# Performance work log

Hardware: AMD Instinct MI355X
Metric: run time of the kernel (lower is better)

Reference implementation:

```python
import math
import jax, jax.numpy as jnp
import numpy as np

D_MODEL, STATE_DIM, SEQ_L = 256, 64, 8192


def setup_inputs() -> dict:
    key = jax.random.key(0)
    ks = jax.random.split(key, 6)
    d, N = D_MODEL, STATE_DIM
    s = 1.0 / math.sqrt(N)
    return {
        "Lambda_re": jax.random.normal(ks[0], (d, N), jnp.float32),
        "Lambda_im": jax.random.normal(ks[1], (d, N), jnp.float32),
        "P_re": jax.random.normal(ks[2], (d, N), jnp.float32) * s,
        "P_im": jax.random.normal(ks[3], (d, N), jnp.float32) * s,
        "B_re": jax.random.normal(ks[4], (d, N), jnp.float32) * s,
        "B_im": jnp.zeros((d, N), jnp.float32),
        "log_dt": jax.random.uniform(ks[5], (d,), jnp.float32,
                                     math.log(1e-3), math.log(0.1)),
        "D": jnp.zeros((d,), jnpp := jnp.float32) if False else jnp.zeros((d,), jnp.float32),
        "L": SEQ_L,
    }


def reference(Lambda_re, Lambda_im, P_re, P_im, B_re, B_im, log_dt, D, L):
    # NPLR / Cauchy-Woodbury S4 kernel (learn_cd=False -> C = B, D is a zero buffer)
    Lam = (-jax.nn.softplus(Lambda_re) + 1j * Lambda_im).astype(jnp.complex64)  # [d, N]
    P = (P_re + 1j * P_im).astype(jnp.complex64)                                # [d, N]
    B = (B_re + 1j * B_im).astype(jnp.complex64)                                # [d, N]
    dt = jnp.exp(log_dt)                                                        # [d]

    k = jnp.arange(L)
    z = jnp.exp((-2j * jnp.pi / L) * k).astype(jnp.complex64)                   # [L] roots of unity
    eps = jnp.finfo(jnp.float32).eps
    denom_z = 1.0 + z
    denom_z = jnp.where(jnp.abs(denom_z) < eps, jnp.complex64(eps), denom_z)

    # Bilinear-transform frequencies g: [d, L] complex
    g = (2.0 / dt)[:, None] * ((1.0 - z) / denom_z)[None, :]

    # Cauchy resolvent R: [d, L, N] complex (the dominant intermediate)
    R = 1.0 / (g[:, :, None] - Lam[:, None, :])

    Pc, Bc = jnp.conj(P), jnp.conj(B)
    PRB = jnp.einsum('dn,dln,dn->dl', Pc, R, B)
    PRP = jnp.einsum('dn,dln,dn->dl', Pc, R, P)
    BRB = jnp.einsum('dn,dln,dn->dl', Bc, R, B)
    BRP = jnp.einsum('dn,dln,dn->dl', Bc, R, P)

    # Woodbury rank-1 correction, then undo the bilinear prefactor
    K_hat = (2.0 / denom_z)[None, :] * (BRB - BRP * PRB / (1.0 + PRP))          # [d, L]
    K = jnp.fft.ifft(K_hat, n=L, axis=-1).real.astype(jnp.float32)
    return (K, D)
```

## Files before the change

### kernel.cpp

```cpp
#include <hip/hip_runtime.h>
#include <math.h>

#ifndef M_PI
#define M_PI 3.14159265358979323846
#endif

#define DMODEL 256
#define NSTATE 64
#define LSEQ   8192
#define INVL   (1.0f/8192.0f)

#define OFF_TW  0
#define OFF_DN  (6144*8)
#define OFF_CDT (OFF_DN + DMODEL*NSTATE*48)
#define OFF_XY  (OFF_CDT + 1024)
#define WS_NEED ((size_t)OFF_XY + (size_t)DMODEL*LSEQ*8)

__device__ __forceinline__ float sin_rev(float r) {
#if __has_builtin(__builtin_amdgcn_sinf)
  return __builtin_amdgcn_sinf(r);
#else
  return __sinf(r * 6.283185307179586f);
#endif
}
__device__ __forceinline__ float cos_rev(float r) {
#if __has_builtin(__builtin_amdgcn_cosf)
  return __builtin_amdgcn_cosf(r);
#else
  return __cosf(r * 6.283185307179586f);
#endif
}

__device__ __forceinline__ float2 cmul(float2 a, float2 b) {
  return make_float2(a.x*b.x - a.y*b.y, a.x*b.y + a.y*b.x);
}

__device__ __forceinline__ float2 woodbury(float2 S1, float2 S2, float2 S3,
                                           float2 S4, float T) {
  float nr = (S1.x*S1.x - S1.y*S1.y) + (S2.x*S2.x - S2.y*S2.y);
  float ni = 2.0f*(S1.x*S1.y + S2.x*S2.y);
  float dr = 1.0f + S3.x, di = S3.y;
  float inv = __builtin_amdgcn_rcpf(fmaf(dr, dr, di*di));
  float qr = (nr*dr + ni*di) * inv;
  float qi = (ni*dr - nr*di) * inv;
  float vr = S4.x - qr, vi = S4.y - qi;
  return make_float2((vr - T*vi)*INVL, (vi + T*vr)*INVL);
}

__device__ __forceinline__ void radix4(float2& x0, float2& x1, float2& x2, float2& x3,
                                       float2 w1, float2 w2, float2 w3) {
  const float2 t1 = cmul(w1, x1);
  const float2 t2 = cmul(w2, x2);
  const float2 t3 = cmul(w3, x3);
  const float2 u0 = make_float2(x0.x + t2.x, x0.y + t2.y);
  const float2 u1 = make_float2(x0.x - t2.x, x0.y - t2.y);
  const float2 u2 = make_float2(t1.x + t3.x, t1.y + t3.y);
  const float2 vv = make_float2(t1.x - t3.x, t1.y - t3.y);
  x0 = make_float2(u0.x + u2.x, u0.y + u2.y);
  x1 = make_float2(u1.x - vv.y, u1.y + vv.x);
  x2 = make_float2(u0.x - u2.x, u0.y - u2.y);
  x3 = make_float2(u1.x + vv.y, u1.y - vv.x);
}

__device__ __forceinline__ float4 cauchy_pair(const float4* __restrict__ dnp,
                                              const float c, const int b) {
  const unsigned p = (unsigned)(2*b);
  const unsigned r = __brev(p) >> 19;
  const int kA = (int)((r & 0x1000u) | ((r & 0x0555u) << 1) | ((r & 0x0AAAu) >> 1));
  const float rev = (float)kA * (1.0f/16384.0f);
  const float sA = sin_rev(rev), cA = cos_rev(rev);
  float TA = sA * __builtin_amdgcn_rcpf(cA);
  float TB = -cA * __builtin_amdgcn_rcpf(sA);
  TA = fminf(fmaxf(TA, -1e7f), 1e7f);
  TB = fminf(fmaxf(TB, -1e7f), 1e7f);
  const float gA = c * TA, gB = c * TB;

  float2 s1a={0,0}, s2a={0,0}, s3a={0,0}, s4a={0,0};
  float2 s1b={0,0}, s2b={0,0}, s3b={0,0}, s4b={0,0};
#pragma unroll 2
  for (int n = 0; n < NSTATE; ++n) {
    const float4 q0 = dnp[3*n];
    const float4 q1 = dnp[3*n+1];
    const float4 q2 = dnp[3*n+2];
    {
      const float dim = q0.x - gA;
      const float inv = __builtin_amdgcn_rcpf(fmaf(dim, dim, q0.y));
      const float v = dim * inv;
      s1a.x = fmaf(q0.z, inv, s1a.x);  s1a.y = fmaf(q1.z, v, s1a.y);
      s2a.x = fmaf(q0.w, inv, s2a.x);  s2a.y = fmaf(q1.w, v, s2a.y);
      s3a.x = fmaf(q1.x, inv, s3a.x);  s3a.y = fmaf(q2.x, v, s3a.y);
      s4a.x = fmaf(q1.y, inv, s4a.x);  s4a.y = fmaf(q2.y, v, s4a.y);
    }
    {
      const float dim = q0.x - gB;
      const float inv = __builtin_amdgcn_rcpf(fmaf(dim, dim, q0.y));
      const float v = dim * inv;
      s1b.x = fmaf(q0.z, inv, s1b.x);  s1b.y = fmaf(q1.z, v, s1b.y);
      s2b.x = fmaf(q0.w, inv, s2b.x);  s2b.y = fmaf(q1.w, v, s2b.y);
      s3b.x = fmaf(q1.x, inv, s3b.x);  s3b.y = fmaf(q2.x, v, s3b.y);
      s4b.x = fmaf(q1.y, inv, s4b.x);  s4b.y = fmaf(q2.y, v, s4b.y);
    }
  }
  const float2 KA = woodbury(s1a, s2a, s3a, s4a, TA);
  const float2 KB = woodbury(s1b, s2b, s3b, s4b, TB);
  return make_float4(KA.x + KB.x, KA.y + KB.y, KA.x - KB.x, KA.y - KB.y);
}

__global__ __launch_bounds__(256) void precompute_kernel(
    const float* __restrict__ Lre, const float* __restrict__ Lim,
    const float* __restrict__ Pre, const float* __restrict__ Pim,
    const float* __restrict__ Bre, const float* __restrict__ Bim,
    const float* __restrict__ log_dt, char* __restrict__ ws)
{
  const int t = blockIdx.x * blockDim.x + threadIdx.x;
  float2* tw  = (float2*)(ws + OFF_TW);
  float4* dn  = (float4*)(ws + OFF_DN);
  float*  cdt = (float*)(ws + OFF_CDT);

  if (t < 6144) {
    double th = (2.0 * M_PI / (double)LSEQ) * (double)t;
    double s, c; sincos(th, &s, &c);
    tw[t] = make_float2((float)c, (float)s);
  }
  {
    float lre = Lre[t], lim = Lim[t];
    float pre = Pre[t], pim = Pim[t];
    float bre = Bre[t], bim = Bim[t];
    float sp = fmaxf(lre, 0.0f) + log1pf(expf(-fabsf(lre)));
    float w1r = pre*bre + pim*bim;
    float w1i = pre*bim - pim*bre;
    float w2  = pre*pre + pim*pim;
    float w3  = bre*bre + bim*bim;
    dn[3*t]   = make_float4(lim, sp*sp, w1r*sp, w1i*sp);
    dn[3*t+1] = make_float4(w2*sp, w3*sp, w1r, w1i);
    dn[3*t+2] = make_float4(w2, w3, 0.0f, 0.0f);
  }
  if (t < DMODEL) cdt[t] = 2.0f * expf(-log_dt[t]);
}

__global__ __launch_bounds__(512, 8) void cauchyfft_kernel(
    const float4* __restrict__ dn_all, const float* __restrict__ cdt,
    const float2* __restrict__ tw, float2* __restrict__ xy_ws)
{
  __shared__ __align__(16) float2 xy[2048];
  const int d   = blockIdx.x >> 2;
  const int seg = blockIdx.x & 3;
  const int t   = threadIdx.x;
  const float c = cdt[d];
  const float4* dnp = dn_all + (size_t)d * (3*NSTATE);

#pragma unroll
  for (int pass = 0; pass < 2; ++pass) {
    const int bl = t + (pass << 9);
    ((float4*)xy)[bl] = cauchy_pair(dnp, c, (seg << 10) + bl);
  }
  __syncthreads();

#pragma unroll
  for (int s = 0; s < 4; ++s) {
    const int h = 2 << (2*s);
    const int twsh = 10 - 2*s;
    const int pos = t & (h - 1);
    const int i0 = ((t >> (1 + 2*s)) << (3 + 2*s)) + pos;
    const int ti = pos << twsh;
    float2 x0 = xy[i0], x1 = xy[i0 + h], x2 = xy[i0 + 2*h], x3 = xy[i0 + 3*h];
    radix4(x0, x1, x2, x3, tw[ti], tw[2*ti], tw[3*ti]);
    xy[i0] = x0; xy[i0 + h] = x1; xy[i0 + 2*h] = x2; xy[i0 + 3*h] = x3;
    __syncthreads();
  }

  {
    const int ti = t << 2;
    float2 x0 = xy[t], x1 = xy[t + 512], x2 = xy[t + 1024], x3 = xy[t + 1536];
    radix4(x0, x1, x2, x3, tw[ti], tw[2*ti], tw[3*ti]);
    float2* xg = xy_ws + (size_t)d * LSEQ + (seg << 11);
    xg[t] = x0; xg[t + 512] = x1; xg[t + 1024] = x2; xg[t + 1536] = x3;
  }
}

__global__ __launch_bounds__(256) void finish_kernel(
    const float2* __restrict__ xy_ws, const float2* __restrict__ tw,
    const float* __restrict__ Din, float* __restrict__ out)
{
  const int d   = blockIdx.x >> 3;
  const int pos = ((blockIdx.x & 7) << 8) + threadIdx.x;
  const float2* xr = xy_ws + (size_t)d * LSEQ;
  const float2 x0 = xr[pos];
  const float2 x1 = xr[pos + 2048];
  const float2 x2 = xr[pos + 4096];
  const float2 x3 = xr[pos + 6144];
  const float2 w1 = tw[pos], w2 = tw[2*pos], w3 = tw[3*pos];
  const float t1x = w1.x*x1.x - w1.y*x1.y, t1y = w1.x*x1.y + w1.y*x1.x;
  const float t2x = w2.x*x2.x - w2.y*x2.y;
  const float t3x = w3.x*x3.x - w3.y*x3.y, t3y = w3.x*x3.y + w3.y*x3.x;
  const float u0 = x0.x + t2x, u1 = x0.x - t2x;
  const float u2 = t1x + t3x, vy = t1y - t3y;
  float* orow = out + (size_t)d * LSEQ;
  orow[pos]        = u0 + u2;
  orow[pos + 2048] = u1 - vy;
  orow[pos + 4096] = u0 - u2;
  orow[pos + 6144] = u1 + vy;

  if (blockIdx.x == 0) out[(size_t)DMODEL * LSEQ + threadIdx.x] =
      (threadIdx.x < DMODEL) ? Din[threadIdx.x] : 0.0f;
}

__global__ __launch_bounds__(1024) void fused_kernel(
    const float4* __restrict__ dn_all, const float* __restrict__ cdt,
    const float2* __restrict__ tw, const float* __restrict__ Din,
    float* __restrict__ out)
{
  __shared__ __align__(16) float2 xy[LSEQ];
  const int d = blockIdx.x;
  const int t = threadIdx.x;
  const float c = cdt[d];
  const float4* dnp = dn_all + (size_t)d * (3*NSTATE);

  for (int j = 0; j < 4; ++j) {
    const int b = t + (j << 10);
    ((float4*)xy)[b] = cauchy_pair(dnp, c, b);
  }
  __syncthreads();

#pragma unroll
  for (int s = 0; s < 6; ++s) {
    const int h = 2 << (2*s);
    const int twsh = 10 - 2*s;
#pragma unroll
    for (int j = 0; j < 2; ++j) {
      const int bb = t + (j << 10);
      const int pos = bb & (h - 1);
      const int i0 = ((bb >> (1 + 2*s)) << (3 + 2*s)) + pos;
      const int ti = pos << twsh;
      float2 x0 = xy[i0], x1 = xy[i0 + h], x2 = xy[i0 + 2*h], x3 = xy[i0 + 3*h];
      radix4(x0, x1, x2, x3, tw[ti], tw[2*ti], tw[3*ti]);
      xy[i0] = x0; xy[i0 + h] = x1; xy[i0 + 2*h] = x2; xy[i0 + 3*h] = x3;
    }
    __syncthreads();
  }

  float* orow = out + (size_t)d * LSEQ;
  for (int i = t; i < LSEQ; i += 1024) orow[i] = xy[i].x;
  if (d == 0 && t < DMODEL) out[(size_t)DMODEL * LSEQ + t] = Din[t];
}

extern "C" void kernel_launch(void* const* d_in, const int* in_sizes, int n_in,
                              void* d_out, int out_size, void* d_ws, size_t ws_size,
                              hipStream_t stream)
{
  const float* Lre    = (const float*)d_in[0];
  const float* Lim    = (const float*)d_in[1];
  const float* Pre    = (const float*)d_in[2];
  const float* Pim    = (const float*)d_in[3];
  const float* Bre    = (const float*)d_in[4];
  const float* Bim    = (const float*)d_in[5];
  const float* log_dt = (const float*)d_in[6];
  const float* Din    = (const float*)d_in[7];
  float* out = (float*)d_out;
  char* ws = (char*)d_ws;

  hipLaunchKernelGGL(precompute_kernel, dim3(64), dim3(256), 0, stream,
                     Lre, Lim, Pre, Pim, Bre, Bim, log_dt, ws);

  if (ws_size >= WS_NEED) {
    hipLaunchKernelGGL(cauchyfft_kernel, dim3(DMODEL * 4), dim3(512), 0, stream,
                       (const float4*)(ws + OFF_DN), (const float*)(ws + OFF_CDT),
                       (const float2*)(ws + OFF_TW), (float2*)(ws + OFF_XY));
    hipLaunchKernelGGL(finish_kernel, dim3(DMODEL * 8), dim3(256), 0, stream,
                       (const float2*)(ws + OFF_XY), (const float2*)(ws + OFF_TW),
                       Din, out);
  } else {
    hipLaunchKernelGGL(fused_kernel, dim3(DMODEL), dim3(1024), 0, stream,
                       (const float4*)(ws + OFF_DN), (const float*)(ws + OFF_CDT),
                       (const float2*)(ws + OFF_TW), Din, out);
  }
}
```

Measured before the change: 128.0 us.

## Fuse both Cauchy passes into one n-loop and swizzle LDS FFT indices

The two per-thread Cauchy evaluations are merged into a single loop over the state dimension, so each dn float4 load is reused for four frequency points instead of two. This halves the global/L1 loads of the dn table and exposes more independent rcp/FMA chains. An XOR swizzle is also applied to the shared-memory FFT buffer indices to cut LDS bank conflicts in the strided radix-4 stages. The cost is higher register pressure from sixteen accumulators, which may lower occupancy under the 512x8 launch bound.

After: 131.3 us. 1.03x slower.

```diff
diff --git a/kernel.cpp b/kernel.cpp
--- a/kernel.cpp
+++ b/kernel.cpp
@@ -15,6 +15,8 @@
 #define OFF_CDT (OFF_DN + DMODEL*NSTATE*48)
 #define OFF_XY  (OFF_CDT + 1024)
 #define WS_NEED ((size_t)OFF_XY + (size_t)DMODEL*LSEQ*8)
+
+#define SWZ(i) ((i) ^ (((i) >> 4) & 14))
 
 __device__ __forceinline__ float sin_rev(float r) {
 #if __has_builtin(__builtin_amdgcn_sinf)
@@ -62,19 +64,25 @@
   x3 = make_float2(u1.x + vv.y, u1.y - vv.x);
 }
 
-__device__ __forceinline__ float4 cauchy_pair(const float4* __restrict__ dnp,
-                                              const float c, const int b) {
+__device__ __forceinline__ void pair_setup(const float c, const int b,
+                                           float& TA, float& TB,
+                                           float& gA, float& gB) {
   const unsigned p = (unsigned)(2*b);
   const unsigned r = __brev(p) >> 19;
   const int kA = (int)((r & 0x1000u) | ((r & 0x0555u) << 1) | ((r & 0x0AAAu) >> 1));
   const float rev = (float)kA * (1.0f/16384.0f);
   const float sA = sin_rev(rev), cA = cos_rev(rev);
-  float TA = sA * __builtin_amdgcn_rcpf(cA);
-  float TB = -cA * __builtin_amdgcn_rcpf(sA);
+  TA = sA * __builtin_amdgcn_rcpf(cA);
+  TB = -cA * __builtin_amdgcn_rcpf(sA);
   TA = fminf(fmaxf(TA, -1e7f), 1e7f);
   TB = fminf(fmaxf(TB, -1e7f), 1e7f);
-  const float gA = c * TA, gB = c * TB;
-
+  gA = c * TA; gB = c * TB;
+}
+
+__device__ __forceinline__ float4 cauchy_pair(const float4* __restrict__ dnp,
+                                              const float c, const int b) {
+  float TA, TB, gA, gB;
+  pair_setup(c, b, TA, TB, gA, gB);
   float2 s1a={0,0}, s2a={0,0}, s3a={0,0}, s4a={0,0};
   float2 s1b={0,0}, s2b={0,0}, s3b={0,0}, s4b={0,0};
 #pragma unroll 2
@@ -149,10 +157,52 @@
   const float c = cdt[d];
   const float4* dnp = dn_all + (size_t)d * (3*NSTATE);
 
-#pragma unroll
-  for (int pass = 0; pass < 2; ++pass) {
-    const int bl = t + (pass << 9);
-    ((float4*)xy)[bl] = cauchy_pair(dnp, c, (seg << 10) + bl);
+  float TA[2], TB[2], gA[2], gB[2];
+  float2 s1[2][2], s2[2][2], s3[2][2], s4[2][2];
+#pragma unroll
+  for (int j = 0; j < 2; ++j) {
+    pair_setup(c, (seg << 10) + t + (j << 9), TA[j], TB[j], gA[j], gB[j]);
+    s1[j][0]=make_float2(0,0); s2[j][0]=make_float2(0,0);
+    s3[j][0]=make_float2(0,0); s4[j][0]=make_float2(0,0);
+    s1[j][1]=make_float2(0,0); s2[j][1]=make_float2(0,0);
+    s3[j][1]=make_float2(0,0); s4[j][1]=make_float2(0,0);
+  }
+
+#pragma unroll 2
+  for (int n = 0; n < NSTATE; ++n) {
+    const float4 q0 = dnp[3*n];
+    const float4 q1 = dnp[3*n+1];
+    const float4 q2 = dnp[3*n+2];
+#pragma unroll
+    for (int j = 0; j < 2; ++j) {
+      {
+        const float dim = q0.x - gA[j];
+        const float inv = __builtin_amdgcn_rcpf(fmaf(dim, dim, q0.y));
+        const float v = dim * inv;
+        s1[j][0].x = fmaf(q0.z, inv, s1[j][0].x);  s1[j][0].y = fmaf(q1.z, v, s1[j][0].y);
+        s2[j][0].x = fmaf(q0.w, inv, s2[j][0].x);  s2[j][0].y = fmaf(q1.w, v, s2[j][0].y);
+        s3[j][0].x = fmaf(q1.x, inv, s3[j][0].x);  s3[j][0].y = fmaf(q2.x, v, s3[j][0].y);
+        s4[j][0].x = fmaf(q1.y, inv, s4[j][0].x);  s4[j][0].y = fmaf(q2.y, v, s4[j][0].y);
+      }
+      {
+        const float dim = q0.x - gB[j];
+        const float inv = __builtin_amdgcn_rcpf(fmaf(dim, dim, q0.y));
+        const float v = dim * inv;
+        s1[j][1].x = fmaf(q0.z, inv, s1[j][1].x);  s1[j][1].y = fmaf(q1.z, v, s1[j][1].y);
+        s2[j][1].x = fmaf(q0.w, inv, s2[j][1].x);  s2[j][1].y = fmaf(q1.w, v, s2[j][1].y);
+        s3[j][1].x = fmaf(q1.x, inv, s3[j][1].x);  s3[j][1].y = fmaf(q2.x, v, s3[j][1].y);
+        s4[j][1].x = fmaf(q1.y, inv, s4[j][1].x);  s4[j][1].y = fmaf(q2.y, v, s4[j][1].y);
+      }
+    }
+  }
+
+#pragma unroll
+  for (int j = 0; j < 2; ++j) {
+    const float2 KA = woodbury(s1[j][0], s2[j][0], s3[j][0], s4[j][0], TA[j]);
+    const float2 KB = woodbury(s1[j][1], s2[j][1], s3[j][1], s4[j][1], TB[j]);
+    const int e0 = 2*(t + (j << 9));
+    ((float4*)xy)[SWZ(e0) >> 1] = make_float4(KA.x + KB.x, KA.y + KB.y,
+                                              KA.x - KB.x, KA.y - KB.y);
   }
   __syncthreads();
 
@@ -163,15 +213,18 @@
     const int pos = t & (h - 1);
     const int i0 = ((t >> (1 + 2*s)) << (3 + 2*s)) + pos;
     const int ti = pos << twsh;
-    float2 x0 = xy[i0], x1 = xy[i0 + h], x2 = xy[i0 + 2*h], x3 = xy[i0 + 3*h];
+    float2 x0 = xy[SWZ(i0)],       x1 = xy[SWZ(i0 + h)];
+    float2 x2 = xy[SWZ(i0 + 2*h)], x3 = xy[SWZ(i0 + 3*h)];
     radix4(x0, x1, x2, x3, tw[ti], tw[2*ti], tw[3*ti]);
-    xy[i0] = x0; xy[i0 + h] = x1; xy[i0 + 2*h] = x2; xy[i0 + 3*h] = x3;
+    xy[SWZ(i0)] = x0;       xy[SWZ(i0 + h)] = x1;
+    xy[SWZ(i0 + 2*h)] = x2; xy[SWZ(i0 + 3*h)] = x3;
     __syncthreads();
   }
 
   {
     const int ti = t << 2;
-    float2 x0 = xy[t], x1 = xy[t + 512], x2 = xy[t + 1024], x3 = xy[t + 1536];
+    float2 x0 = xy[SWZ(t)],        x1 = xy[SWZ(t + 512)];
+    float2 x2 = xy[SWZ(t + 1024)], x3 = xy[SWZ(t + 1536)];
     radix4(x0, x1, x2, x3, tw[ti], tw[2*ti], tw[3*ti]);
     float2* xg = xy_ws + (size_t)d * LSEQ + (seg << 11);
     xg[t] = x0; xg[t + 512] = x1; xg[t + 1024] = x2; xg[t + 1536] = x3;
```

## Stage Cauchy coefficients in LDS, swizzle FFT shared memory, vectorize finish kernel

Applied to the files above, without the earlier changes.

The per-channel Cauchy coefficient table is copied into shared memory once per block, and the inner loop's unroll factor goes from 2 to 4. The shared FFT buffer indices are XOR-swizzled to cut LDS bank conflicts in the radix-4 stages. The finish kernel now handles two adjacent positions per thread with float4 loads and float2 stores, so it launches half as many blocks. Together these aim to reduce global-load and LDS traffic, at the cost of an extra barrier and more register pressure from the deeper unroll.

Measured after the change: 129.9 us. About the same (+1.5%).

```diff
diff --git a/kernel.cpp b/kernel.cpp
--- a/kernel.cpp
+++ b/kernel.cpp
@@ -15,6 +15,8 @@
 #define OFF_CDT (OFF_DN + DMODEL*NSTATE*48)
 #define OFF_XY  (OFF_CDT + 1024)
 #define WS_NEED ((size_t)OFF_XY + (size_t)DMODEL*LSEQ*8)
+
+#define SWZ(i) ((i) ^ ((((i) >> 4) & 7) << 1))
 
 __device__ __forceinline__ float sin_rev(float r) {
 #if __has_builtin(__builtin_amdgcn_sinf)
@@ -62,22 +64,29 @@
   x3 = make_float2(u1.x + vv.y, u1.y - vv.x);
 }
 
-__device__ __forceinline__ float4 cauchy_pair(const float4* __restrict__ dnp,
-                                              const float c, const int b) {
+__device__ __forceinline__ void pair_setup(const float c, const int b,
+                                           float& TA, float& TB,
+                                           float& gA, float& gB) {
   const unsigned p = (unsigned)(2*b);
   const unsigned r = __brev(p) >> 19;
   const int kA = (int)((r & 0x1000u) | ((r & 0x0555u) << 1) | ((r & 0x0AAAu) >> 1));
   const float rev = (float)kA * (1.0f/16384.0f);
   const float sA = sin_rev(rev), cA = cos_rev(rev);
-  float TA = sA * __builtin_amdgcn_rcpf(cA);
-  float TB = -cA * __builtin_amdgcn_rcpf(sA);
+  TA = sA * __builtin_amdgcn_rcpf(cA);
+  TB = -cA * __builtin_amdgcn_rcpf(sA);
   TA = fminf(fmaxf(TA, -1e7f), 1e7f);
   TB = fminf(fmaxf(TB, -1e7f), 1e7f);
-  const float gA = c * TA, gB = c * TB;
-
+  gA = c * TA; gB = c * TB;
+}
+
+template <typename TQ>
+__device__ __forceinline__ float4 cauchy_pair_tab(const TQ* dnp,
+                                                  const float c, const int b) {
+  float TA, TB, gA, gB;
+  pair_setup(c, b, TA, TB, gA, gB);
   float2 s1a={0,0}, s2a={0,0}, s3a={0,0}, s4a={0,0};
   float2 s1b={0,0}, s2b={0,0}, s3b={0,0}, s4b={0,0};
-#pragma unroll 2
+#pragma unroll 4
   for (int n = 0; n < NSTATE; ++n) {
     const float4 q0 = dnp[3*n];
     const float4 q1 = dnp[3*n+1];
@@ -143,16 +152,22 @@
     const float2* __restrict__ tw, float2* __restrict__ xy_ws)
 {
   __shared__ __align__(16) float2 xy[2048];
+  __shared__ __align__(16) float4 dnl[3*NSTATE];
   const int d   = blockIdx.x >> 2;
   const int seg = blockIdx.x & 3;
   const int t   = threadIdx.x;
   const float c = cdt[d];
   const float4* dnp = dn_all + (size_t)d * (3*NSTATE);
 
+  if (t < 3*NSTATE) dnl[t] = dnp[t];
+  __syncthreads();
+
 #pragma unroll
   for (int pass = 0; pass < 2; ++pass) {
     const int bl = t + (pass << 9);
-    ((float4*)xy)[bl] = cauchy_pair(dnp, c, (seg << 10) + bl);
+    const float4 K2 = cauchy_pair_tab(dnl, c, (seg << 10) + bl);
+    const int e0 = 2*bl;
+    ((float4*)xy)[SWZ(e0) >> 1] = K2;
   }
   __syncthreads();
 
@@ -163,15 +178,18 @@
     const int pos = t & (h - 1);
     const int i0 = ((t >> (1 + 2*s)) << (3 + 2*s)) + pos;
     const int ti = pos << twsh;
-    float2 x0 = xy[i0], x1 = xy[i0 + h], x2 = xy[i0 + 2*h], x3 = xy[i0 + 3*h];
+    float2 x0 = xy[SWZ(i0)],       x1 = xy[SWZ(i0 + h)];
+    float2 x2 = xy[SWZ(i0 + 2*h)], x3 = xy[SWZ(i0 + 3*h)];
     radix4(x0, x1, x2, x3, tw[ti], tw[2*ti], tw[3*ti]);
-    xy[i0] = x0; xy[i0 + h] = x1; xy[i0 + 2*h] = x2; xy[i0 + 3*h] = x3;
+    xy[SWZ(i0)] = x0;       xy[SWZ(i0 + h)] = x1;
+    xy[SWZ(i0 + 2*h)] = x2; xy[SWZ(i0 + 3*h)] = x3;
     __syncthreads();
   }
 
   {
     const int ti = t << 2;
-    float2 x0 = xy[t], x1 = xy[t + 512], x2 = xy[t + 1024], x3 = xy[t + 1536];
+    float2 x0 = xy[SWZ(t)],        x1 = xy[SWZ(t + 512)];
+    float2 x2 = xy[SWZ(t + 1024)], x3 = xy[SWZ(t + 1536)];
     radix4(x0, x1, x2, x3, tw[ti], tw[2*ti], tw[3*ti]);
     float2* xg = xy_ws + (size_t)d * LSEQ + (seg << 11);
     xg[t] = x0; xg[t + 512] = x1; xg[t + 1024] = x2; xg[t + 1536] = x3;
@@ -182,27 +200,45 @@
     const float2* __restrict__ xy_ws, const float2* __restrict__ tw,
     const float* __restrict__ Din, float* __restrict__ out)
 {
-  const int d   = blockIdx.x >> 3;
-  const int pos = ((blockIdx.x & 7) << 8) + threadIdx.x;
-  const float2* xr = xy_ws + (size_t)d * LSEQ;
-  const float2 x0 = xr[pos];
-  const float2 x1 = xr[pos + 2048];
-  const float2 x2 = xr[pos + 4096];
-  const float2 x3 = xr[pos + 6144];
-  const float2 w1 = tw[pos], w2 = tw[2*pos], w3 = tw[3*pos];
-  const float t1x = w1.x*x1.x - w1.y*x1.y, t1y = w1.x*x1.y + w1.y*x1.x;
-  const float t2x = w2.x*x2.x - w2.y*x2.y;
-  const float t3x = w3.x*x3.x - w3.y*x3.y, t3y = w3.x*x3.y + w3.y*x3.x;
-  const float u0 = x0.x + t2x, u1 = x0.x - t2x;
-  const float u2 = t1x + t3x, vy = t1y - t3y;
-  float* orow = out + (size_t)d * LSEQ;
-  orow[pos]        = u0 + u2;
-  orow[pos + 2048] = u1 - vy;
-  orow[pos + 4096] = u0 - u2;
-  orow[pos + 6144] = u1 + vy;
-
-  if (blockIdx.x == 0) out[(size_t)DMODEL * LSEQ + threadIdx.x] =
-      (threadIdx.x < DMODEL) ? Din[threadIdx.x] : 0.0f;
+  const int d  = blockIdx.x >> 2;
+  const int p2 = ((blockIdx.x & 3) << 8) + threadIdx.x;
+  const float4* xr4 = (const float4*)(xy_ws + (size_t)d * LSEQ);
+  const float4* tw4 = (const float4*)tw;
+  const float4 X0 = xr4[p2];
+  const float4 X1 = xr4[p2 + 1024];
+  const float4 X2 = xr4[p2 + 2048];
+  const float4 X3 = xr4[p2 + 3072];
+  const float4 W1  = tw4[p2];
+  const float4 W2a = tw4[2*p2];
+  const float4 W2b = tw4[2*p2 + 1];
+  const float4 W3a = tw4[3*p2];
+  const float4 W3b = tw4[3*p2 + 1];
+
+  float y0[2], y1[2], y2[2], y3[2];
+#pragma unroll
+  for (int u = 0; u < 2; ++u) {
+    const float2 x0 = u ? make_float2(X0.z, X0.w) : make_float2(X0.x, X0.y);
+    const float2 x1 = u ? make_float2(X1.z, X1.w) : make_float2(X1.x, X1.y);
+    const float2 x2 = u ? make_float2(X2.z, X2.w) : make_float2(X2.x, X2.y);
+    const float2 x3 = u ? make_float2(X3.z, X3.w) : make_float2(X3.x, X3.y);
+    const float2 w1 = u ? make_float2(W1.z, W1.w) : make_float2(W1.x, W1.y);
+    const float2 w2 = u ? make_float2(W2b.x, W2b.y) : make_float2(W2a.x, W2a.y);
+    const float2 w3 = u ? make_float2(W3b.z, W3b.w) : make_float2(W3a.x, W3a.y);
+    const float t1x = w1.x*x1.x - w1.y*x1.y, t1y = w1.x*x1.y + w1.y*x1.x;
+    const float t2x = w2.x*x2.x - w2.y*x2.y;
+    const float t3x = w3.x*x3.x - w3.y*x3.y, t3y = w3.x*x3.y + w3.y*x3.x;
+    const float u0 = x0.x + t2x, u1 = x0.x - t2x;
+    const float u2 = t1x + t3x, vy = t1y - t3y;
+    y0[u] = u0 + u2; y1[u] = u1 - vy; y2[u] = u0 - u2; y3[u] = u1 + vy;
+  }
+  float2* orow2 = (float2*)(out + (size_t)d * LSEQ);
+  orow2[p2]        = make_float2(y0[0], y0[1]);
+  orow2[p2 + 1024] = make_float2(y1[0], y1[1]);
+  orow2[p2 + 2048] = make_float2(y2[0], y2[1]);
+  orow2[p2 + 3072] = make_float2(y3[0], y3[1]);
+
+  if (blockIdx.x == 0 && threadIdx.x < DMODEL)
+    out[(size_t)DMODEL * LSEQ + threadIdx.x] = Din[threadIdx.x];
 }
 
 __global__ __launch_bounds__(1024) void fused_kernel(
@@ -218,7 +254,7 @@
 
   for (int j = 0; j < 4; ++j) {
     const int b = t + (j << 10);
-    ((float4*)xy)[b] = cauchy_pair(dnp, c, b);
+    ((float4*)xy)[b] = cauchy_pair_tab(dnp, c, b);
   }
   __syncthreads();
 
@@ -266,7 +302,7 @@
     hipLaunchKernelGGL(cauchyfft_kernel, dim3(DMODEL * 4), dim3(512), 0, stream,
                        (const float4*)(ws + OFF_DN), (const float*)(ws + OFF_CDT),
                        (const float2*)(ws + OFF_TW), (float2*)(ws + OFF_XY));
-    hipLaunchKernelGGL(finish_kernel, dim3(DMODEL * 8), dim3(256), 0, stream,
+    hipLaunchKernelGGL(finish_kernel, dim3(DMODEL * 4), dim3(256), 0, stream,
                        (const float2*)(ws + OFF_XY), (const float2*)(ws + OFF_TW),
                        Din, out);
   } else {
```
